# Optimization experiments

Measured on AMD Instinct MI355X. Metric: run time of the kernel, lower is better.

Reference implementation:

```python
import jax, jax.numpy as jnp
import numpy as np

EPS = 1e-5
NEG_SLOPE = 0.01  # torch F.leaky_relu default


def _batchnorm(h, gamma, beta):
    # BatchNorm1d in training mode: batch stats over node dim, biased variance
    mu = jnp.mean(h, axis=0)
    var = jnp.mean((h - mu) ** 2, axis=0)
    return gamma * (h - mu) * jax.lax.rsqrt(var + EPS) + beta


def setup_inputs() -> dict:
    N, E, H, ED = 16384, 524288, 128, 16
    key = jax.random.key(0)
    ks = jax.random.split(key, 12)
    s = 1.0 / np.sqrt(H)
    return {
        "x": jax.random.normal(ks[0], (N, H), jnp.float32),
        "edge_index": jax.random.randint(ks[1], (2, E), 0, N, jnp.int64),
        "edge_attr": jax.random.normal(ks[2], (E, ED), jnp.float32),
        "Wq": jax.random.normal(ks[3], (H, H), jnp.float32) * s,
        "bq": jnp.zeros((H,), jnp.float32),
        "Wk": jax.random.normal(ks[4], (H, H), jnp.float32) * s,
        "bk": jnp.zeros((H,), jnp.float32),
        "Wv": jax.random.normal(ks[5], (H, H), jnp.float32) * s,
        "bv": jnp.zeros((H,), jnp.float32),
        "We": jax.random.normal(ks[6], (ED, 1), jnp.float32) * (1.0 / np.sqrt(ED)),
        "be": jnp.zeros((1,), jnp.float32),
        "bn1_g": jnp.ones((H,), jnp.float32),
        "bn1_b": jnp.zeros((H,), jnp.float32),
        "W1": jax.random.normal(ks[7], (H, 2 * H), jnp.float32) * s,
        "b1": jnp.zeros((2 * H,), jnp.float32),
        "W2": jax.random.normal(ks[8], (2 * H, H), jnp.float32) * (1.0 / np.sqrt(2 * H)),
        "b2": jnp.zeros((H,), jnp.float32),
        "bn2_g": jnp.ones((H,), jnp.float32),
        "bn2_b": jnp.zeros((H,), jnp.float32),
    }


def reference(x, edge_index, edge_attr, Wq, bq, Wk, bk, Wv, bv, We, be,
              bn1_g, bn1_b, W1, b1, W2, b2, bn2_g, bn2_b):
    N = x.shape[0]
    Q = x @ Wq + bq  # [N, H]
    K = x @ Wk + bk
    V = x @ Wv + bv
    Ebias = (edge_attr @ We + be)[:, 0]  # [E], num_heads == 1
    src, dst = edge_index[0], edge_index[1]
    # per-edge dot product over the FULL hidden dim (as in the source)
    scores = jnp.sum(Q[src] * K[dst], axis=1) + Ebias  # [E]
    scores = jnp.where(scores >= 0, scores, NEG_SLOPE * scores)
    # to_dense_adj scatter-adds edge_attr into a dense [N, N] adjacency
    adj = jnp.zeros((N, N), x.dtype).at[src, dst].add(scores)
    attn = jax.nn.softmax(adj, axis=1)  # dense softmax incl. zero non-edges
    x_new = attn @ V  # [N, H]
    h = _batchnorm(x + x_new, bn1_g, bn1_b)
    ffn = jax.nn.relu(h @ W1 + b1) @ W2 + b2
    return _batchnorm(h + ffn, bn2_g, bn2_b)
```

## Files before the change

kernel.cpp:

```cpp
#include <hip/hip_runtime.h>
#include <hip/hip_bf16.h>
#include <math.h>

#define H 128
#define H2 256
#define SLAB 96
#define LDA 136
#define LDA2 264
#define EPS 1e-5f

typedef __attribute__((ext_vector_type(8))) short s16x8;
typedef __attribute__((ext_vector_type(4))) float f32x4;

__device__ __forceinline__ unsigned short f2bf(float f) {
  unsigned u = __float_as_uint(f);
  unsigned r = (u + 0x7FFFu + ((u >> 16) & 1u)) >> 16;
  return (unsigned short)r;
}
__device__ __forceinline__ float bf2f(unsigned short s) {
  return __uint_as_float(((unsigned)s) << 16);
}
__device__ __forceinline__ unsigned short f2h(float f) {
  union { unsigned short s; _Float16 h; } c; c.h = (_Float16)f; return c.s;
}
__device__ __forceinline__ float h2f(unsigned short u) {
  union { unsigned short s; _Float16 h; } c; c.s = u; return (float)c.h;
}

__global__ void wprep(const float* __restrict__ Wq, const float* __restrict__ Wk,
                      const float* __restrict__ Wv, const float* __restrict__ W1,
                      const float* __restrict__ W2,
                      short* qh, short* kh, short* vh, short* w1h, short* w2h,
                      int* __restrict__ cnt, float* __restrict__ stats, int N)
{
  int job = blockIdx.z;
  if (job == 5) {
    int t = blockIdx.x * 256 + threadIdx.x;
    if (t < N) cnt[t] = 0;
    if (t < 72 * H) stats[t] = 0.f;
    return;
  }
  const float* src; short* dh; int Kd, Nn; bool ashalf;
  if (job == 0)      { src = Wq; dh = qh;  Kd = 128; Nn = 128; ashalf = true; }
  else if (job == 1) { src = Wk; dh = kh;  Kd = 128; Nn = 128; ashalf = true; }
  else if (job == 2) { src = Wv; dh = vh;  Kd = 128; Nn = 128; ashalf = true; }
  else if (job == 3) { src = W1; dh = w1h; Kd = 128; Nn = 256; ashalf = false; }
  else               { src = W2; dh = w2h; Kd = 256; Nn = 128; ashalf = false; }
  int t = blockIdx.x * 256 + threadIdx.x;
  if (t >= Kd * Nn) return;
  int n = t / Kd, k = t - n * Kd;
  float v = src[(size_t)k * Nn + n];
  dh[t] = ashalf ? (short)f2h(v) : (short)f2bf(v);
}

__global__ __launch_bounds__(256) void qkv_mfma(
    const float* __restrict__ x,
    const short* __restrict__ Wqh, const short* __restrict__ Wkh,
    const short* __restrict__ Wvh,
    const float* __restrict__ bq, const float* __restrict__ bk,
    const float* __restrict__ bv,
    unsigned short* __restrict__ Qh, unsigned short* __restrict__ Kh,
    unsigned short* __restrict__ Vh, float* __restrict__ SVp,
    const float* __restrict__ ea, const float* __restrict__ We,
    const float* __restrict__ be, float* __restrict__ Eb,
    int E, int nqkv)
{
  __shared__ __align__(16) short A[64 * LDA];
  int tid = threadIdx.x;

  if (blockIdx.x >= nqkv) {
    int e = (blockIdx.x - nqkv) * 256 + tid;
    if (e < E) {
      float4 w0 = *(const float4*)&We[0], w1 = *(const float4*)&We[4];
      float4 w2 = *(const float4*)&We[8], w3 = *(const float4*)&We[12];
      const float4* p = (const float4*)&ea[(size_t)e * 16];
      float4 a0 = p[0], a1 = p[1], a2 = p[2], a3 = p[3];
      float s = a0.x * w0.x + a0.y * w0.y + a0.z * w0.z + a0.w * w0.w
              + a1.x * w1.x + a1.y * w1.y + a1.z * w1.z + a1.w * w1.w
              + a2.x * w2.x + a2.y * w2.y + a2.z * w2.z + a2.w * w2.w
              + a3.x * w3.x + a3.y * w3.y + a3.z * w3.z + a3.w * w3.w;
      Eb[e] = s + be[0];
    }
    return;
  }

  int bm = blockIdx.x * 64;
  int wave = tid >> 6, lane = tid & 63;
  int quad = lane >> 4, l16 = lane & 15;
  int wn = wave * 32;

#pragma unroll
  for (int i = 0; i < 4; ++i) {
    int g = i * 256 + tid;
    int row = g >> 4, f = g & 15;
    const float4* xp = (const float4*)&x[(size_t)(bm + row) * H + f * 8];
    float4 v0 = xp[0], v1 = xp[1];
    float vv[8] = {v0.x, v0.y, v0.z, v0.w, v1.x, v1.y, v1.z, v1.w};
    s16x8 hv;
#pragma unroll
    for (int j = 0; j < 8; ++j) hv[j] = (short)f2h(vv[j]);
    *(s16x8*)&A[row * LDA + f * 8] = hv;
  }
  __syncthreads();

  for (int ph = 0; ph < 3; ++ph) {
    const short* Bh = (ph == 0) ? Wqh : (ph == 1) ? Wkh : Wvh;

    s16x8 bh[2][4];
#pragma unroll
    for (int nt = 0; nt < 2; ++nt)
#pragma unroll
      for (int ks = 0; ks < 4; ++ks)
        bh[nt][ks] = *(const s16x8*)&Bh[(size_t)(wn + nt * 16 + l16) * H + ks * 32 + quad * 8];

    f32x4 acc[4][2];
#pragma unroll
    for (int mt = 0; mt < 4; ++mt)
#pragma unroll
      for (int nt = 0; nt < 2; ++nt) acc[mt][nt] = (f32x4){0.f, 0.f, 0.f, 0.f};

#pragma unroll
    for (int ks = 0; ks < 4; ++ks) {
      int kof = ks * 32 + quad * 8;
      s16x8 ah[4];
#pragma unroll
      for (int mt = 0; mt < 4; ++mt)
        ah[mt] = *(s16x8*)&A[(mt * 16 + l16) * LDA + kof];
#pragma unroll
      for (int mt = 0; mt < 4; ++mt)
#pragma unroll
        for (int nt = 0; nt < 2; ++nt)
          acc[mt][nt] = __builtin_amdgcn_mfma_f32_16x16x32_f16(ah[mt], bh[nt][ks], acc[mt][nt], 0, 0, 0);
    }

    if (ph == 0) {
#pragma unroll
      for (int nt = 0; nt < 2; ++nt) {
        int col = wn + nt * 16 + l16;
        float bb = bq[col];
#pragma unroll
        for (int mt = 0; mt < 4; ++mt)
#pragma unroll
          for (int r = 0; r < 4; ++r) {
            int row = bm + mt * 16 + quad * 4 + r;
            Qh[(size_t)row * H + col] = f2h(acc[mt][nt][r] + bb);
          }
      }
    } else if (ph == 1) {
#pragma unroll
      for (int nt = 0; nt < 2; ++nt) {
        int col = wn + nt * 16 + l16;
        float bb = bk[col];
#pragma unroll
        for (int mt = 0; mt < 4; ++mt)
#pragma unroll
          for (int r = 0; r < 4; ++r) {
            int row = bm + mt * 16 + quad * 4 + r;
            Kh[(size_t)row * H + col] = f2h(acc[mt][nt][r] + bb);
          }
      }
    } else {
      int bank = blockIdx.x & 7;
#pragma unroll
      for (int nt = 0; nt < 2; ++nt) {
        int col = wn + nt * 16 + l16;
        float bb = bv[col];
        float ps = 0.f;
#pragma unroll
        for (int mt = 0; mt < 4; ++mt)
#pragma unroll
          for (int r = 0; r < 4; ++r) {
            int row = bm + mt * 16 + quad * 4 + r;
            float v = acc[mt][nt][r] + bb;
            Vh[(size_t)row * H + col] = f2h(v);
            ps += v;
          }
        ps += __shfl_xor(ps, 16);
        ps += __shfl_xor(ps, 32);
        if (quad == 0) atomicAdd(&SVp[bank * H + col], ps);
      }
    }
  }
}

__global__ __launch_bounds__(256) void ebfill(
    const int* __restrict__ ei,
    const float* __restrict__ Eb,
    const unsigned short* __restrict__ Qh,
    const unsigned short* __restrict__ Kh,
    int* __restrict__ cnt,
    int2* __restrict__ slabDE, int E, int N)
{
  __shared__ int qeP[2048];
  __shared__ float qeB[2048];
  __shared__ int qn;
  int tid = threadIdx.x;
  int grp = blockIdx.x & 7;
  int blk = blockIdx.x >> 3;
  int lo = grp * (N >> 3), hi = lo + (N >> 3);
  int per = E >> 8;
  int base = blk * per;
  const int* eiD = ei + E;

  if (tid == 0) qn = 0;
  __syncthreads();

  for (int i = 0; i < per; i += 256) {
    int e = base + i + tid;
    if (e >= E) continue;
    int src = ei[e];
    int dst = eiD[e];
    float b = Eb[e];
    if (src >= lo && src < hi) {
      int p = atomicAdd(&qn, 1);
      qeP[p] = (dst << 11) | (src - lo);
      qeB[p] = b;
    }
  }
  __syncthreads();

  int m = qn;
  int sub = tid & 7, st = tid >> 3;
  int j = st;
  for (; j + 32 < m; j += 64) {
    int pA = qeP[j], pB = qeP[j + 32];
    float bA = qeB[j], bB = qeB[j + 32];
    int sA = lo + (pA & 2047), dA = pA >> 11;
    int sB = lo + (pB & 2047), dB = pB >> 11;
    const s16x8* qpA = (const s16x8*)(Qh + (size_t)sA * H);
    const s16x8* kpA = (const s16x8*)(Kh + (size_t)dA * H);
    const s16x8* qpB = (const s16x8*)(Qh + (size_t)sB * H);
    const s16x8* kpB = (const s16x8*)(Kh + (size_t)dB * H);
    s16x8 qa0 = qpA[sub], qb0 = qpA[8 + sub];
    s16x8 ka0 = kpA[sub], kb0 = kpA[8 + sub];
    s16x8 qa1 = qpB[sub], qb1 = qpB[8 + sub];
    s16x8 ka1 = kpB[sub], kb1 = kpB[8 + sub];
    float s0 = 0.f, s1 = 0.f;
#pragma unroll
    for (int u = 0; u < 8; ++u) {
      s0 += h2f((unsigned short)qa0[u]) * h2f((unsigned short)ka0[u]);
      s0 += h2f((unsigned short)qb0[u]) * h2f((unsigned short)kb0[u]);
      s1 += h2f((unsigned short)qa1[u]) * h2f((unsigned short)ka1[u]);
      s1 += h2f((unsigned short)qb1[u]) * h2f((unsigned short)kb1[u]);
    }
    s0 += __shfl_xor(s0, 1); s1 += __shfl_xor(s1, 1);
    s0 += __shfl_xor(s0, 2); s1 += __shfl_xor(s1, 2);
    s0 += __shfl_xor(s0, 4); s1 += __shfl_xor(s1, 4);
    if (sub == 0) {
      s0 += bA; s1 += bB;
      s0 = (s0 >= 0.f) ? s0 : 0.01f * s0;
      s1 = (s1 >= 0.f) ? s1 : 0.01f * s1;
      int posA = atomicAdd(&cnt[sA], 1);
      if (posA < SLAB) {
        int2 rec; rec.x = dA; rec.y = __float_as_int(s0);
        slabDE[sA * SLAB + posA] = rec;
      }
      int posB = atomicAdd(&cnt[sB], 1);
      if (posB < SLAB) {
        int2 rec; rec.x = dB; rec.y = __float_as_int(s1);
        slabDE[sB * SLAB + posB] = rec;
      }
    }
  }
  for (; j < m; j += 32) {
    int p = qeP[j];
    float b = qeB[j];
    int src = lo + (p & 2047), dst = p >> 11;
    const s16x8* qp = (const s16x8*)(Qh + (size_t)src * H);
    const s16x8* kp = (const s16x8*)(Kh + (size_t)dst * H);
    s16x8 qa = qp[sub], qb = qp[8 + sub];
    s16x8 ka = kp[sub], kb = kp[8 + sub];
    float s = 0.f;
#pragma unroll
    for (int u = 0; u < 8; ++u) {
      s += h2f((unsigned short)qa[u]) * h2f((unsigned short)ka[u]);
      s += h2f((unsigned short)qb[u]) * h2f((unsigned short)kb[u]);
    }
    s += __shfl_xor(s, 1);
    s += __shfl_xor(s, 2);
    s += __shfl_xor(s, 4);
    if (sub == 0) {
      s += b;
      s = (s >= 0.f) ? s : 0.01f * s;
      int pos = atomicAdd(&cnt[src], 1);
      if (pos < SLAB) {
        int2 rec; rec.x = dst; rec.y = __float_as_int(s);
        slabDE[src * SLAB + pos] = rec;
      }
    }
  }
}

__global__ __launch_bounds__(256) void attn_fused(
    const float* __restrict__ x,
    const unsigned short* __restrict__ Vh,
    const float* __restrict__ SVp, const int* __restrict__ cnt,
    const int2* __restrict__ slabDE,
    float* __restrict__ h1, float* __restrict__ sum1p, float* __restrict__ sq1p,
    int N)
{
  __shared__ float sv[4][SLAB];
  __shared__ int sd[4][SLAB];
  __shared__ short sown[4][SLAB];
  __shared__ float csum[H], csq[H];
  int tid = threadIdx.x;
  int team = tid >> 6, lane = tid & 63;
  int grp = blockIdx.x & 7;
  int r = blockIdx.x >> 3;
  int i = grp * (N >> 3) + r * 4 + team;
  int k = cnt[i]; if (k > SLAB) k = SLAB;
  int base = i * SLAB;

  if (tid < H) { csum[tid] = 0.f; csq[tid] = 0.f; }
  __syncthreads();

  for (int p = lane; p < k; p += 64) {
    int2 de = slabDE[base + p];
    sd[team][p] = de.x;
    sv[team][p] = __int_as_float(de.y);
  }

  for (int p = lane; p < k; p += 64) {
    int d = sd[team][p];
    int o = p;
    for (int q = p - 1; q >= 0; --q)
      o = (sd[team][q] == d) ? q : o;
    sown[team][p] = (short)o;
  }
  for (int p = lane; p < k; p += 64) {
    int o = sown[team][p];
    if (o != p) atomicAdd(&sv[team][o], sv[team][p]);
  }

  float mx = 0.f;
  for (int p = lane; p < k; p += 64)
    if (sown[team][p] == (short)p) mx = fmaxf(mx, sv[team][p]);
#pragma unroll
  for (int msk = 32; msk; msk >>= 1) mx = fmaxf(mx, __shfl_xor(mx, msk));
  float em = __expf(-mx);

  float zl = 0.f;
  for (int p = lane; p < k; p += 64) {
    float cf = 0.f;
    if (sown[team][p] == (short)p) cf = __expf(sv[team][p] - mx) - em;
    sv[team][p] = cf;
    zl += cf;
  }
#pragma unroll
  for (int msk = 32; msk; msk >>= 1) zl += __shfl_xor(zl, msk);
  float Zi = 1.f / ((float)N * em + zl);

  float sx = 0.f, sy = 0.f;
#pragma unroll
  for (int b = 0; b < 8; ++b) {
    float2 t = *(const float2*)&SVp[b * H + lane * 2];
    sx += t.x; sy += t.y;
  }

  const ushort2* V2 = (const ushort2*)Vh;
  float ax = em * sx, ay = em * sy;
  int c = 0;
  for (; c + 8 <= k; c += 8) {
    float cf[8]; int dd[8]; ushort2 vv[8];
#pragma unroll
    for (int u = 0; u < 8; ++u) { cf[u] = sv[team][c + u]; dd[u] = sd[team][c + u]; }
#pragma unroll
    for (int u = 0; u < 8; ++u) vv[u] = V2[(size_t)dd[u] * 64 + lane];
#pragma unroll
    for (int u = 0; u < 8; ++u) {
      ax += cf[u] * h2f(vv[u].x);
      ay += cf[u] * h2f(vv[u].y);
    }
  }
  for (; c < k; ++c) {
    float cf = sv[team][c];
    ushort2 v0 = V2[(size_t)sd[team][c] * 64 + lane];
    ax += cf * h2f(v0.x); ay += cf * h2f(v0.y);
  }
  float2 xx = *(const float2*)&x[(size_t)i * H + lane * 2];
  float ox = xx.x + ax * Zi;
  float oy = xx.y + ay * Zi;
  float2 ov; ov.x = ox; ov.y = oy;
  *(float2*)&h1[(size_t)i * H + lane * 2] = ov;

  int c0 = lane * 2;
  atomicAdd(&csum[c0 + 0], ox); atomicAdd(&csq[c0 + 0], ox * ox);
  atomicAdd(&csum[c0 + 1], oy); atomicAdd(&csq[c0 + 1], oy * oy);
  __syncthreads();
  if (tid < H) {
    int bank = blockIdx.x & 15;
    atomicAdd(&sum1p[bank * H + tid], csum[tid]);
    atomicAdd(&sq1p[bank * H + tid], csq[tid]);
  }
}

__global__ __launch_bounds__(256) void ffn_fused(
    const float* __restrict__ h1, const short* __restrict__ W1h,
    const float* __restrict__ b1, const short* __restrict__ W2h,
    const float* __restrict__ b2,
    const float* __restrict__ sum1p, const float* __restrict__ sq1p,
    const float* __restrict__ g1, const float* __restrict__ bb1,
    float* __restrict__ h2, float* __restrict__ sum2p, float* __restrict__ sq2p,
    float invN)
{
  __shared__ __align__(16) short As[32 * LDA];
  __shared__ __align__(16) short Ts[32 * LDA2];
  __shared__ float aF[H], bF[H];
  int tid = threadIdx.x;
  int bm = blockIdx.x * 32;
  int wave = tid >> 6, lane = tid & 63;
  int quad = lane >> 4, l16 = lane & 15;

  if (tid < H) {
    float s = 0.f, q = 0.f;
#pragma unroll
    for (int b = 0; b < 16; ++b) { s += sum1p[b * H + tid]; q += sq1p[b * H + tid]; }
    float mu = s * invN;
    float var = q * invN - mu * mu;
    float rs = rsqrtf(var + EPS);
    float a = g1[tid] * rs;
    aF[tid] = a;
    bF[tid] = bb1[tid] - a * mu;
  }
  __syncthreads();

  int f = tid & 15;
#pragma unroll
  for (int i = 0; i < 2; ++i) {
    int g = i * 256 + tid;
    int row = g >> 4;
    const float4* xp = (const float4*)&h1[(size_t)(bm + row) * H + f * 8];
    float4 v0 = xp[0], v1 = xp[1];
    float vv[8] = {v0.x, v0.y, v0.z, v0.w, v1.x, v1.y, v1.z, v1.w};
    s16x8 hv;
#pragma unroll
    for (int j = 0; j < 8; ++j) {
      int c = f * 8 + j;
      hv[j] = (short)f2bf(aF[c] * vv[j] + bF[c]);
    }
    *(s16x8*)&As[row * LDA + f * 8] = hv;
  }

  int wn1 = wave * 64;
  s16x8 b1f[4][4];
#pragma unroll
  for (int nt = 0; nt < 4; ++nt)
#pragma unroll
    for (int ks = 0; ks < 4; ++ks)
      b1f[nt][ks] = *(const s16x8*)&W1h[(size_t)(wn1 + nt * 16 + l16) * H + ks * 32 + quad * 8];
  __syncthreads();

  f32x4 acc1[2][4];
#pragma unroll
  for (int mt = 0; mt < 2; ++mt)
#pragma unroll
    for (int nt = 0; nt < 4; ++nt) acc1[mt][nt] = (f32x4){0.f, 0.f, 0.f, 0.f};

#pragma unroll
  for (int ks = 0; ks < 4; ++ks) {
    int kof = ks * 32 + quad * 8;
    s16x8 ah[2];
#pragma unroll
    for (int mt = 0; mt < 2; ++mt) ah[mt] = *(s16x8*)&As[(mt * 16 + l16) * LDA + kof];
#pragma unroll
    for (int mt = 0; mt < 2; ++mt)
#pragma unroll
      for (int nt = 0; nt < 4; ++nt)
        acc1[mt][nt] = __builtin_amdgcn_mfma_f32_16x16x32_bf16(ah[mt], b1f[nt][ks], acc1[mt][nt], 0, 0, 0);
  }

#pragma unroll
  for (int nt = 0; nt < 4; ++nt) {
    int col = wn1 + nt * 16 + l16;
    float bb = b1[col];
#pragma unroll
    for (int mt = 0; mt < 2; ++mt)
#pragma unroll
      for (int r = 0; r < 4; ++r) {
        int row = mt * 16 + quad * 4 + r;
        float v = acc1[mt][nt][r] + bb;
        v = v > 0.f ? v : 0.f;
        Ts[row * LDA2 + col] = (short)f2bf(v);
      }
  }

  int wn2 = wave * 32;
  s16x8 b2f[2][8];
#pragma unroll
  for (int nt = 0; nt < 2; ++nt)
#pragma unroll
    for (int ks = 0; ks < 8; ++ks)
      b2f[nt][ks] = *(const s16x8*)&W2h[(size_t)(wn2 + nt * 16 + l16) * H2 + ks * 32 + quad * 8];
  __syncthreads();

  f32x4 acc2[2][2];
#pragma unroll
  for (int mt = 0; mt < 2; ++mt)
#pragma unroll
    for (int nt = 0; nt < 2; ++nt) acc2[mt][nt] = (f32x4){0.f, 0.f, 0.f, 0.f};

#pragma unroll
  for (int ks = 0; ks < 8; ++ks) {
    int kof = ks * 32 + quad * 8;
    s16x8 ah[2];
#pragma unroll
    for (int mt = 0; mt < 2; ++mt) ah[mt] = *(s16x8*)&Ts[(mt * 16 + l16) * LDA2 + kof];
#pragma unroll
    for (int mt = 0; mt < 2; ++mt)
#pragma unroll
      for (int nt = 0; nt < 2; ++nt)
        acc2[mt][nt] = __builtin_amdgcn_mfma_f32_16x16x32_bf16(ah[mt], b2f[nt][ks], acc2[mt][nt], 0, 0, 0);
  }

  int bank = blockIdx.x & 15;
#pragma unroll
  for (int nt = 0; nt < 2; ++nt) {
    int col = wn2 + nt * 16 + l16;
    float ra = aF[col], rb = bF[col];
    float bb = b2[col];
    float ps = 0.f, pq = 0.f;
#pragma unroll
    for (int mt = 0; mt < 2; ++mt)
#pragma unroll
      for (int r = 0; r < 4; ++r) {
        int row = bm + mt * 16 + quad * 4 + r;
        float rr = ra * h1[(size_t)row * H + col] + rb;
        float v = acc2[mt][nt][r] + bb + rr;
        h2[(size_t)row * H + col] = v;
        ps += v; pq += v * v;
      }
    ps += __shfl_xor(ps, 16); ps += __shfl_xor(ps, 32);
    pq += __shfl_xor(pq, 16); pq += __shfl_xor(pq, 32);
    if (quad == 0) {
      atomicAdd(&sum2p[bank * H + col], ps);
      atomicAdd(&sq2p[bank * H + col], pq);
    }
  }
}

__global__ __launch_bounds__(256) void bn_apply(
    const float* __restrict__ X,
    const float* __restrict__ sum2p, const float* __restrict__ sq2p,
    const float* __restrict__ g2, const float* __restrict__ bb2,
    float* __restrict__ Y, size_t n4, float invN)
{
  __shared__ float A2s[H], B2s[H];
  int tid = threadIdx.x;
  if (tid < H) {
    float s = 0.f, q = 0.f;
#pragma unroll
    for (int b = 0; b < 16; ++b) { s += sum2p[b * H + tid]; q += sq2p[b * H + tid]; }
    float mu = s * invN;
    float var = q * invN - mu * mu;
    float rs = rsqrtf(var + EPS);
    float a = g2[tid] * rs;
    A2s[tid] = a;
    B2s[tid] = bb2[tid] - a * mu;
  }
  __syncthreads();
  size_t i = (size_t)blockIdx.x * blockDim.x + tid;
  if (i >= n4) return;
  float4 v = ((const float4*)X)[i];
  int c = (int)((i * 4) & (H - 1));
  float4 a = *(const float4*)&A2s[c];
  float4 b = *(const float4*)&B2s[c];
  v.x = a.x * v.x + b.x; v.y = a.y * v.y + b.y;
  v.z = a.z * v.z + b.z; v.w = a.w * v.w + b.w;
  ((float4*)Y)[i] = v;
}

extern "C" void kernel_launch(void* const* d_in, const int* in_sizes, int n_in,
                              void* d_out, int out_size, void* d_ws, size_t ws_size,
                              hipStream_t stream)
{
  const float* x  = (const float*)d_in[0];
  const int*   ei = (const int*)d_in[1];
  const float* ea = (const float*)d_in[2];
  const float* Wq = (const float*)d_in[3];
  const float* bq = (const float*)d_in[4];
  const float* Wk = (const float*)d_in[5];
  const float* bk = (const float*)d_in[6];
  const float* Wv = (const float*)d_in[7];
  const float* bv = (const float*)d_in[8];
  const float* We = (const float*)d_in[9];
  const float* be = (const float*)d_in[10];
  const float* g1 = (const float*)d_in[11];
  const float* bb1 = (const float*)d_in[12];
  const float* W1 = (const float*)d_in[13];
  const float* b1 = (const float*)d_in[14];
  const float* W2 = (const float*)d_in[15];
  const float* b2 = (const float*)d_in[16];
  const float* g2 = (const float*)d_in[17];
  const float* bb2 = (const float*)d_in[18];

  int N = in_sizes[0] / H;
  int E = in_sizes[2] / 16;
  size_t NH = (size_t)N * H;
  float invN = 1.0f / (float)N;

  unsigned short* Qh = (unsigned short*)d_ws;
  unsigned short* Kh = Qh + NH;
  unsigned short* Vh = Kh + NH;
  float* h1  = (float*)(Vh + NH);
  int2*  slabDE = (int2*)(h1 + NH);
  int*   cnt    = (int*)(slabDE + (size_t)N * SLAB);
  float* stats  = (float*)(cnt + N);
  float* SVp   = stats;
  float* sum1p = stats + 8 * H;
  float* sq1p  = sum1p + 16 * H;
  float* sum2p = sq1p + 16 * H;
  float* sq2p  = sum2p + 16 * H;
  float* statsEnd = sq2p + 16 * H;
  short* wbuf = (short*)statsEnd;
  short* Wqf = wbuf;
  short* Wkf = Wqf + 16384;
  short* Wvf = Wkf + 16384;
  short* W1h = Wvf + 16384;
  short* W2h = W1h + 32768;
  float* Eb  = (float*)(W2h + 32768);
  float* h2 = (float*)Qh;

  int nqkv = N / 64;
  int nebias = (E + 255) / 256;

  wprep<<<dim3(128, 1, 6), 256, 0, stream>>>(Wq, Wk, Wv, W1, W2,
      Wqf, Wkf, Wvf, W1h, W2h, cnt, stats, N);

  qkv_mfma<<<dim3(nqkv + nebias), 256, 0, stream>>>(
      x, Wqf, Wkf, Wvf, bq, bk, bv, Qh, Kh, Vh, SVp,
      ea, We, be, Eb, E, nqkv);

  ebfill<<<dim3(2048), 256, 0, stream>>>(ei, Eb, Qh, Kh, cnt, slabDE, E, N);

  attn_fused<<<dim3(N / 4), 256, 0, stream>>>(x, Vh, SVp, cnt, slabDE,
                                              h1, sum1p, sq1p, N);

  ffn_fused<<<dim3(N / 32), 256, 0, stream>>>(h1, W1h, b1, W2h, b2,
      sum1p, sq1p, g1, bb1, h2, sum2p, sq2p, invN);

  bn_apply<<<dim3((int)((NH / 4 + 255) / 256)), 256, 0, stream>>>(
      h2, sum2p, sq2p, g2, bb2, (float*)d_out, NH / 4, invN);
}
```

Baseline: 219.5 us.

## Hash-table duplicate detection and deeper unrolling of edge gather loops

The edge-score kernel now handles four edges per 8-lane group per iteration instead of two, so more Q/K gathers are in flight at once. In attn_fused, the quadratic backward scan that finds duplicate destinations is replaced by a per-team 128-entry shared-memory hash table with atomicCAS and linear probing. The x and SVp loads are hoisted earlier to overlap with the dedup work, and the V gather loop gains a 16-wide unrolled stage. These changes add register pressure and a shared-memory table, and hash probing can serialise under collisions.

```diff
diff --git a/kernel.cpp b/kernel.cpp
--- a/kernel.cpp
+++ b/kernel.cpp
@@ -222,43 +222,47 @@
   int m = qn;
   int sub = tid & 7, st = tid >> 3;
   int j = st;
-  for (; j + 32 < m; j += 64) {
-    int pA = qeP[j], pB = qeP[j + 32];
-    float bA = qeB[j], bB = qeB[j + 32];
-    int sA = lo + (pA & 2047), dA = pA >> 11;
-    int sB = lo + (pB & 2047), dB = pB >> 11;
-    const s16x8* qpA = (const s16x8*)(Qh + (size_t)sA * H);
-    const s16x8* kpA = (const s16x8*)(Kh + (size_t)dA * H);
-    const s16x8* qpB = (const s16x8*)(Qh + (size_t)sB * H);
-    const s16x8* kpB = (const s16x8*)(Kh + (size_t)dB * H);
-    s16x8 qa0 = qpA[sub], qb0 = qpA[8 + sub];
-    s16x8 ka0 = kpA[sub], kb0 = kpA[8 + sub];
-    s16x8 qa1 = qpB[sub], qb1 = qpB[8 + sub];
-    s16x8 ka1 = kpB[sub], kb1 = kpB[8 + sub];
-    float s0 = 0.f, s1 = 0.f;
-#pragma unroll
-    for (int u = 0; u < 8; ++u) {
-      s0 += h2f((unsigned short)qa0[u]) * h2f((unsigned short)ka0[u]);
-      s0 += h2f((unsigned short)qb0[u]) * h2f((unsigned short)kb0[u]);
-      s1 += h2f((unsigned short)qa1[u]) * h2f((unsigned short)ka1[u]);
-      s1 += h2f((unsigned short)qb1[u]) * h2f((unsigned short)kb1[u]);
-    }
-    s0 += __shfl_xor(s0, 1); s1 += __shfl_xor(s1, 1);
-    s0 += __shfl_xor(s0, 2); s1 += __shfl_xor(s1, 2);
-    s0 += __shfl_xor(s0, 4); s1 += __shfl_xor(s1, 4);
+  for (; j + 96 < m; j += 128) {
+    int pP[4]; float bP[4]; int sP[4], dP[4];
+#pragma unroll
+    for (int u = 0; u < 4; ++u) {
+      pP[u] = qeP[j + u * 32];
+      bP[u] = qeB[j + u * 32];
+      sP[u] = lo + (pP[u] & 2047);
+      dP[u] = pP[u] >> 11;
+    }
+    s16x8 qa[4], qb[4], ka[4], kb[4];
+#pragma unroll
+    for (int u = 0; u < 4; ++u) {
+      const s16x8* qp = (const s16x8*)(Qh + (size_t)sP[u] * H);
+      const s16x8* kp = (const s16x8*)(Kh + (size_t)dP[u] * H);
+      qa[u] = qp[sub]; qb[u] = qp[8 + sub];
+      ka[u] = kp[sub]; kb[u] = kp[8 + sub];
+    }
+    float s[4] = {0.f, 0.f, 0.f, 0.f};
+#pragma unroll
+    for (int u = 0; u < 4; ++u)
+#pragma unroll
+      for (int v = 0; v < 8; ++v) {
+        s[u] += h2f((unsigned short)qa[u][v]) * h2f((unsigned short)ka[u][v]);
+        s[u] += h2f((unsigned short)qb[u][v]) * h2f((unsigned short)kb[u][v]);
+      }
+#pragma unroll
+    for (int u = 0; u < 4; ++u) {
+      s[u] += __shfl_xor(s[u], 1);
+      s[u] += __shfl_xor(s[u], 2);
+      s[u] += __shfl_xor(s[u], 4);
+    }
     if (sub == 0) {
-      s0 += bA; s1 += bB;
-      s0 = (s0 >= 0.f) ? s0 : 0.01f * s0;
-      s1 = (s1 >= 0.f) ? s1 : 0.01f * s1;
-      int posA = atomicAdd(&cnt[sA], 1);
-      if (posA < SLAB) {
-        int2 rec; rec.x = dA; rec.y = __float_as_int(s0);
-        slabDE[sA * SLAB + posA] = rec;
-      }
-      int posB = atomicAdd(&cnt[sB], 1);
-      if (posB < SLAB) {
-        int2 rec; rec.x = dB; rec.y = __float_as_int(s1);
-        slabDE[sB * SLAB + posB] = rec;
+#pragma unroll
+      for (int u = 0; u < 4; ++u) {
+        float ss = s[u] + bP[u];
+        ss = (ss >= 0.f) ? ss : 0.01f * ss;
+        int pos = atomicAdd(&cnt[sP[u]], 1);
+        if (pos < SLAB) {
+          int2 rec; rec.x = dP[u]; rec.y = __float_as_int(ss);
+          slabDE[sP[u] * SLAB + pos] = rec;
+        }
       }
     }
   }
@@ -302,6 +306,7 @@
   __shared__ float sv[4][SLAB];
   __shared__ int sd[4][SLAB];
   __shared__ short sown[4][SLAB];
+  __shared__ int tab[4][128];
   __shared__ float csum[H], csq[H];
   int tid = threadIdx.x;
   int team = tid >> 6, lane = tid & 63;
@@ -312,6 +317,8 @@
   int base = i * SLAB;
 
   if (tid < H) { csum[tid] = 0.f; csq[tid] = 0.f; }
+  tab[team][lane] = -1;
+  tab[team][lane + 64] = -1;
   __syncthreads();
 
   for (int p = lane; p < k; p += 64) {
@@ -320,11 +327,24 @@
     sv[team][p] = __int_as_float(de.y);
   }
 
+  float2 xx = *(const float2*)&x[(size_t)i * H + lane * 2];
+  float sx = 0.f, sy = 0.f;
+#pragma unroll
+  for (int b = 0; b < 8; ++b) {
+    float2 t = *(const float2*)&SVp[b * H + lane * 2];
+    sx += t.x; sy += t.y;
+  }
+
   for (int p = lane; p < k; p += 64) {
     int d = sd[team][p];
-    int o = p;
-    for (int q = p - 1; q >= 0; --q)
-      o = (sd[team][q] == d) ? q : o;
+    unsigned hsh = ((unsigned)d * 2654435761u) >> 25;
+    int o;
+    while (true) {
+      int old = atomicCAS(&tab[team][hsh & 127], -1, p);
+      if (old == -1) { o = p; break; }
+      if (sd[team][old] == d) { o = old; break; }
+      ++hsh;
+    }
     sown[team][p] = (short)o;
   }
   for (int p = lane; p < k; p += 64) {
@@ -350,16 +370,21 @@
   for (int msk = 32; msk; msk >>= 1) zl += __shfl_xor(zl, msk);
   float Zi = 1.f / ((float)N * em + zl);
 
-  float sx = 0.f, sy = 0.f;
-#pragma unroll
-  for (int b = 0; b < 8; ++b) {
-    float2 t = *(const float2*)&SVp[b * H + lane * 2];
-    sx += t.x; sy += t.y;
-  }
-
   const ushort2* V2 = (const ushort2*)Vh;
   float ax = em * sx, ay = em * sy;
   int c = 0;
+  for (; c + 16 <= k; c += 16) {
+    float cf[16]; int dd[16]; ushort2 vv[16];
+#pragma unroll
+    for (int u = 0; u < 16; ++u) { cf[u] = sv[team][c + u]; dd[u] = sd[team][c + u]; }
+#pragma unroll
+    for (int u = 0; u < 16; ++u) vv[u] = V2[(size_t)dd[u] * 64 + lane];
+#pragma unroll
+    for (int u = 0; u < 16; ++u) {
+      ax += cf[u] * h2f(vv[u].x);
+      ay += cf[u] * h2f(vv[u].y);
+    }
+  }
   for (; c + 8 <= k; c += 8) {
     float cf[8]; int dd[8]; ushort2 vv[8];
 #pragma unroll
@@ -377,7 +402,6 @@
     ushort2 v0 = V2[(size_t)sd[team][c] * 64 + lane];
     ax += cf * h2f(v0.x); ay += cf * h2f(v0.y);
   }
-  float2 xx = *(const float2*)&x[(size_t)i * H + lane * 2];
   float ox = xx.x + ax * Zi;
   float oy = xx.y + ay * Zi;
   float2 ov; ov.x = ox; ov.y = oy;
```

New measurement: 225.9 us. 1.03x slower.

## Stream edges directly in ebfill, hash-dedup destinations, deepen V gather unroll

Applied to the files above, without the earlier changes.

The edge-scoring kernel no longer buckets edges into shared-memory queues by source range. Each 8-lane subgroup now grid-strides directly over edges, two at a time. The attention kernel replaces the quadratic per-row duplicate-destination search with a shared-memory open-addressing hash table built with atomicCAS. It also hoists the x and SVp loads earlier and adds a 16-wide unrolled V gather loop. This removes the staging pass and the O(k^2) scan, but gives up the source-range locality of slab writes and Q reads, and the grid mapping of both kernels changes.

```diff
diff --git a/kernel.cpp b/kernel.cpp
--- a/kernel.cpp
+++ b/kernel.cpp
@@ -191,42 +191,21 @@
     int* __restrict__ cnt,
     int2* __restrict__ slabDE, int E, int N)
 {
-  __shared__ int qeP[2048];
-  __shared__ float qeB[2048];
-  __shared__ int qn;
   int tid = threadIdx.x;
-  int grp = blockIdx.x & 7;
-  int blk = blockIdx.x >> 3;
-  int lo = grp * (N >> 3), hi = lo + (N >> 3);
-  int per = E >> 8;
-  int base = blk * per;
+  int sub = tid & 7, st = tid >> 3;
+  int gsub = blockIdx.x * 32 + st;
+  int nsub = gridDim.x * 32;
   const int* eiD = ei + E;
 
-  if (tid == 0) qn = 0;
-  __syncthreads();
-
-  for (int i = 0; i < per; i += 256) {
-    int e = base + i + tid;
-    if (e >= E) continue;
-    int src = ei[e];
-    int dst = eiD[e];
-    float b = Eb[e];
-    if (src >= lo && src < hi) {
-      int p = atomicAdd(&qn, 1);
-      qeP[p] = (dst << 11) | (src - lo);
-      qeB[p] = b;
-    }
-  }
-  __syncthreads();
-
-  int m = qn;
-  int sub = tid & 7, st = tid >> 3;
-  int j = st;
-  for (; j + 32 < m; j += 64) {
-    int pA = qeP[j], pB = qeP[j + 32];
-    float bA = qeB[j], bB = qeB[j + 32];
-    int sA = lo + (pA & 2047), dA = pA >> 11;
-    int sB = lo + (pB & 2047), dB = pB >> 11;
+  for (int e = gsub; e < E; e += 2 * nsub) {
+    int eA = e, eB = e + nsub;
+    bool hasB = (eB < E);
+    int sA = ei[eA], dA = eiD[eA];
+    float bA = Eb[eA];
+    int sB = hasB ? ei[eB] : sA;
+    int dB = hasB ? eiD[eB] : dA;
+    float bB = hasB ? Eb[eB] : 0.f;
+
     const s16x8* qpA = (const s16x8*)(Qh + (size_t)sA * H);
     const s16x8* kpA = (const s16x8*)(Kh + (size_t)dA * H);
     const s16x8* qpB = (const s16x8*)(Qh + (size_t)sB * H);
@@ -247,45 +226,21 @@
     s0 += __shfl_xor(s0, 2); s1 += __shfl_xor(s1, 2);
     s0 += __shfl_xor(s0, 4); s1 += __shfl_xor(s1, 4);
     if (sub == 0) {
-      s0 += bA; s1 += bB;
+      s0 += bA;
       s0 = (s0 >= 0.f) ? s0 : 0.01f * s0;
-      s1 = (s1 >= 0.f) ? s1 : 0.01f * s1;
       int posA = atomicAdd(&cnt[sA], 1);
       if (posA < SLAB) {
         int2 rec; rec.x = dA; rec.y = __float_as_int(s0);
-        slabDE[sA * SLAB + posA] = rec;
+        slabDE[(size_t)sA * SLAB + posA] = rec;
       }
-      int posB = atomicAdd(&cnt[sB], 1);
-      if (posB < SLAB) {
-        int2 rec; rec.x = dB; rec.y = __float_as_int(s1);
-        slabDE[sB * SLAB + posB] = rec;
-      }
-    }
-  }
-  for (; j < m; j += 32) {
-    int p = qeP[j];
-    float b = qeB[j];
-    int src = lo + (p & 2047), dst = p >> 11;
-    const s16x8* qp = (const s16x8*)(Qh + (size_t)src * H);
-    const s16x8* kp = (const s16x8*)(Kh + (size_t)dst * H);
-    s16x8 qa = qp[sub], qb = qp[8 + sub];
-    s16x8 ka = kp[sub], kb = kp[8 + sub];
-    float s = 0.f;
-#pragma unroll
-    for (int u = 0; u < 8; ++u) {
-      s += h2f((unsigned short)qa[u]) * h2f((unsigned short)ka[u]);
-      s += h2f((unsigned short)qb[u]) * h2f((unsigned short)kb[u]);
-    }
-    s += __shfl_xor(s, 1);
-    s += __shfl_xor(s, 2);
-    s += __shfl_xor(s, 4);
-    if (sub == 0) {
-      s += b;
-      s = (s >= 0.f) ? s : 0.01f * s;
-      int pos = atomicAdd(&cnt[src], 1);
-      if (pos < SLAB) {
-        int2 rec; rec.x = dst; rec.y = __float_as_int(s);
-        slabDE[src * SLAB + pos] = rec;
+      if (hasB) {
+        s1 += bB;
+        s1 = (s1 >= 0.f) ? s1 : 0.01f * s1;
+        int posB = atomicAdd(&cnt[sB], 1);
+        if (posB < SLAB) {
+          int2 rec; rec.x = dB; rec.y = __float_as_int(s1);
+          slabDE[(size_t)sB * SLAB + posB] = rec;
+        }
       }
     }
   }
@@ -302,16 +257,17 @@
   __shared__ float sv[4][SLAB];
   __shared__ int sd[4][SLAB];
   __shared__ short sown[4][SLAB];
+  __shared__ int tab[4][128];
   __shared__ float csum[H], csq[H];
   int tid = threadIdx.x;
   int team = tid >> 6, lane = tid & 63;
-  int grp = blockIdx.x & 7;
-  int r = blockIdx.x >> 3;
-  int i = grp * (N >> 3) + r * 4 + team;
+  int i = blockIdx.x * 4 + team;
   int k = cnt[i]; if (k > SLAB) k = SLAB;
-  int base = i * SLAB;
+  size_t base = (size_t)i * SLAB;
 
   if (tid < H) { csum[tid] = 0.f; csq[tid] = 0.f; }
+  tab[team][lane] = -1;
+  tab[team][lane + 64] = -1;
   __syncthreads();
 
   for (int p = lane; p < k; p += 64) {
@@ -320,11 +276,24 @@
     sv[team][p] = __int_as_float(de.y);
   }
 
+  float2 xx = *(const float2*)&x[(size_t)i * H + lane * 2];
+  float sx = 0.f, sy = 0.f;
+#pragma unroll
+  for (int b = 0; b < 8; ++b) {
+    float2 t = *(const float2*)&SVp[b * H + lane * 2];
+    sx += t.x; sy += t.y;
+  }
+
   for (int p = lane; p < k; p += 64) {
     int d = sd[team][p];
-    int o = p;
-    for (int q = p - 1; q >= 0; --q)
-      o = (sd[team][q] == d) ? q : o;
+    unsigned hsh = ((unsigned)d * 2654435761u) >> 25;
+    int o;
+    while (true) {
+      int old = atomicCAS(&tab[team][hsh & 127], -1, p);
+      if (old == -1) { o = p; break; }
+      if (sd[team][old] == d) { o = old; break; }
+      ++hsh;
+    }
     sown[team][p] = (short)o;
   }
   for (int p = lane; p < k; p += 64) {
@@ -350,16 +319,21 @@
   for (int msk = 32; msk; msk >>= 1) zl += __shfl_xor(zl, msk);
   float Zi = 1.f / ((float)N * em + zl);
 
-  float sx = 0.f, sy = 0.f;
-#pragma unroll
-  for (int b = 0; b < 8; ++b) {
-    float2 t = *(const float2*)&SVp[b * H + lane * 2];
-    sx += t.x; sy += t.y;
-  }
-
   const ushort2* V2 = (const ushort2*)Vh;
   float ax = em * sx, ay = em * sy;
   int c = 0;
+  for (; c + 16 <= k; c += 16) {
+    float cf[16]; int dd[16]; ushort2 vv[16];
+#pragma unroll
+    for (int u = 0; u < 16; ++u) { cf[u] = sv[team][c + u]; dd[u] = sd[team][c + u]; }
+#pragma unroll
+    for (int u = 0; u < 16; ++u) vv[u] = V2[(size_t)dd[u] * 64 + lane];
+#pragma unroll
+    for (int u = 0; u < 16; ++u) {
+      ax += cf[u] * h2f(vv[u].x);
+      ay += cf[u] * h2f(vv[u].y);
+    }
+  }
   for (; c + 8 <= k; c += 8) {
     float cf[8]; int dd[8]; ushort2 vv[8];
 #pragma unroll
@@ -377,7 +351,6 @@
     ushort2 v0 = V2[(size_t)sd[team][c] * 64 + lane];
     ax += cf * h2f(v0.x); ay += cf * h2f(v0.y);
   }
-  float2 xx = *(const float2*)&x[(size_t)i * H + lane * 2];
   float ox = xx.x + ax * Zi;
   float oy = xx.y + ay * Zi;
   float2 ov; ov.x = ox; ov.y = oy;
```

New measurement: 222.0 us. About the same (+1.1%).
